# Kernel tuning notes

Measured on AMD Instinct MI355X. Metric: run time of the kernel, lower is better.

## Reference

```python
import jax, jax.numpy as jnp
import numpy as np
from jax import lax

K = 3
ALPHA = 2000.0
TAU = 0.001
MAX_ITER = 100
EPS = 1e-7


def setup_inputs() -> dict:
    key = jax.random.key(0)
    x = jax.random.normal(key, (8, 2048, 32), dtype=jnp.float32)
    return {"x": x}


def _vmd(x):
    B, L, D = x.shape
    # shifted frequency grid, identical across B and D
    f = jnp.fft.fftshift(jnp.fft.fftfreq(L)).astype(x.dtype)          # [L]
    f_bld = f[None, :, None]                                           # [1,L,1]
    # nonnegative-frequency mask; torch code boolean-masks f_shifted >= 0,
    # which is uniform over B and D, so it is a weighted sum over L here
    pos = (f >= 0).astype(x.dtype)[None, None, :, None]                # [1,1,L,1]
    x_hat = jnp.fft.fftshift(jnp.fft.fft(x, axis=1), axes=1)          # [B,L,D] complex

    def step(carry, _):
        u, omega, lam = carry  # u:[B,K,L,D], omega:[B,K,D], lam:[B,L,D]
        # Gauss-Seidel mode updates (each mode sees already-updated others)
        for k_idx in range(K):
            sum_other = jnp.sum(u, axis=1) - u[:, k_idx]               # [B,L,D]
            sum_other_hat = jnp.fft.fftshift(jnp.fft.fft(sum_other, axis=1), axes=1)
            num = x_hat - sum_other_hat + lam * 0.5                    # lam added in freq domain, as in source
            den = 1.0 + 2.0 * ALPHA * (f_bld - omega[:, k_idx][:, None, :]) ** 2
            u_k = jnp.real(jnp.fft.ifft(jnp.fft.ifftshift(num / den, axes=1), axis=1))
            u = u.at[:, k_idx].set(u_k)
        # center-frequency update over nonnegative shifted frequencies
        u_hat = jnp.fft.fftshift(jnp.fft.fft(u, axis=2), axes=2)       # [B,K,L,D]
        p = (u_hat.real ** 2 + u_hat.imag ** 2) * pos                  # |u_hat|^2 masked
        omega = jnp.sum(f[None, None, :, None] * p, axis=2) / (jnp.sum(p, axis=2) + EPS)  # [B,K,D]
        # dual ascent on lambda
        lam = lam + TAU * (x - jnp.sum(u, axis=1))
        return (u, omega, lam), None

    u0 = jnp.zeros((B, K, L, D), x.dtype)
    om0 = jnp.zeros((B, K, D), x.dtype)
    lam0 = jnp.zeros((B, L, D), x.dtype)
    (u, omega, _), _ = lax.scan(jax.checkpoint(step), (u0, om0, lam0), None, length=MAX_ITER)

    # sort modes per batch element by mean center frequency
    order = jnp.argsort(jnp.mean(omega, axis=2), axis=1)               # [B,K]
    u_sorted = jnp.take_along_axis(u, order[:, :, None, None], axis=1)
    return u_sorted[:, 0], u_sorted[:, 1], u_sorted[:, 2]


def reference(x):
    return _vmd(x)
```

## Files before the change

### kernel.cpp

```cpp
#include <hip/hip_runtime.h>

#define PD(i) ((i) + ((i) >> 5))
#define BLD 524288

__device__ __forceinline__ float2 cadd(float2 a, float2 b){ return make_float2(a.x+b.x, a.y+b.y); }
__device__ __forceinline__ float2 csub(float2 a, float2 b){ return make_float2(a.x-b.x, a.y-b.y); }
__device__ __forceinline__ float2 cmul(float2 a, float2 b){ return make_float2(a.x*b.x - a.y*b.y, a.x*b.y + a.y*b.x); }
__device__ __forceinline__ float2 cmuli(float2 a, float s){ return make_float2(-s*a.y, s*a.x); }

template<int SGN>
__device__ __forceinline__ void dft8(float2 a[8]) {
  const float sgn = (float)SGN;
  const float C8 = 0.70710678118654752440f;
  float2 e0=a[0], e1=a[2], e2=a[4], e3=a[6];
  float2 o0=a[1], o1=a[3], o2=a[5], o3=a[7];
  float2 t0=cadd(e0,e2), t1=csub(e0,e2), t2=cadd(e1,e3), t3=csub(e1,e3);
  float2 E0=cadd(t0,t2), E2=csub(t0,t2);
  float2 t3i=cmuli(t3,sgn);
  float2 E1=cadd(t1,t3i), E3=csub(t1,t3i);
  float2 s0=cadd(o0,o2), s1=csub(o0,o2), s2=cadd(o1,o3), s3=csub(o1,o3);
  float2 O0=cadd(s0,s2), O2=csub(s0,s2);
  float2 s3i=cmuli(s3,sgn);
  float2 O1=cadd(s1,s3i), O3=csub(s1,s3i);
  float2 w1o = make_float2(C8*(O1.x - sgn*O1.y), C8*(O1.y + sgn*O1.x));
  float2 w2o = cmuli(O2, sgn);
  float2 w3o = make_float2(-C8*(O3.x + sgn*O3.y), C8*(sgn*O3.x - O3.y));
  a[0]=cadd(E0,O0); a[4]=csub(E0,O0);
  a[1]=cadd(E1,w1o); a[5]=csub(E1,w1o);
  a[2]=cadd(E2,w2o); a[6]=csub(E2,w2o);
  a[3]=cadd(E3,w3o); a[7]=csub(E3,w3o);
}

template<int SGN>
__device__ void fft2048(float2* bufA, float2* bufB, const float2* twd, int tid)
{
  const float sgn = (float)SGN;
  {
    float2 a[8];
    #pragma unroll
    for (int j=0;j<8;j++) a[j] = bufA[PD(tid + 256*j)];
    dft8<SGN>(a);
    float2 tw = twd[tid];
    float2 w1 = make_float2(tw.x, sgn*tw.y), wj = w1;
    #pragma unroll
    for (int j=1;j<8;j++){ a[j] = cmul(a[j], wj); wj = cmul(wj, w1); }
    #pragma unroll
    for (int j=0;j<8;j++) bufB[PD(8*tid + j)] = a[j];
  }
  __syncthreads();
  {
    float2 a[8];
    #pragma unroll
    for (int j=0;j<8;j++) a[j] = bufB[PD(tid + 256*j)];
    dft8<SGN>(a);
    int p = tid >> 3, q = tid & 7;
    float2 tw = twd[p << 3];
    float2 w1 = make_float2(tw.x, sgn*tw.y), wj = w1;
    #pragma unroll
    for (int j=1;j<8;j++){ a[j] = cmul(a[j], wj); wj = cmul(wj, w1); }
    int base = q + (p << 6);
    #pragma unroll
    for (int j=0;j<8;j++) bufA[PD(base + (j<<3))] = a[j];
  }
  __syncthreads();
  {
    float2 a[8];
    #pragma unroll
    for (int j=0;j<8;j++) a[j] = bufA[PD(tid + 256*j)];
    dft8<SGN>(a);
    int p = tid >> 6, q = tid & 63;
    float2 tw = twd[p << 6];
    float2 w1 = make_float2(tw.x, sgn*tw.y), wj = w1;
    #pragma unroll
    for (int j=1;j<8;j++){ a[j] = cmul(a[j], wj); wj = cmul(wj, w1); }
    int base = q + (p << 9);
    #pragma unroll
    for (int j=0;j<8;j++) bufB[PD(base + (j<<6))] = a[j];
  }
  __syncthreads();
  {
    #pragma unroll
    for (int h=0; h<2; h++){
      int q = tid + (h<<8);
      float2 b0 = bufB[PD(q)], b1 = bufB[PD(q+512)], b2 = bufB[PD(q+1024)], b3 = bufB[PD(q+1536)];
      float2 t0=cadd(b0,b2), t1=csub(b0,b2), t2=cadd(b1,b3), t3=csub(b1,b3);
      float2 t3i=cmuli(t3,sgn);
      bufA[PD(q)]      = cadd(t0,t2);
      bufA[PD(q+512)]  = cadd(t1,t3i);
      bufA[PD(q+1024)] = csub(t0,t2);
      bufA[PD(q+1536)] = csub(t1,t3i);
    }
  }
  __syncthreads();
}

__device__ __forceinline__ void dft4p(float2 a[4]){
  float2 t0=cadd(a[0],a[2]), t1=csub(a[0],a[2]), t2=cadd(a[1],a[3]), t3=csub(a[1],a[3]);
  float2 t3i = make_float2(-t3.y, t3.x);
  a[0]=cadd(t0,t2); a[2]=csub(t0,t2);
  a[1]=cadd(t1,t3i); a[3]=csub(t1,t3i);
}

template<int S, int LS>
__device__ __forceinline__ void f1024_stage(const float2* __restrict__ in,
                                            float2* __restrict__ out,
                                            const float2* __restrict__ twd, int tid){
  float2 a[4];
  #pragma unroll
  for (int j=0;j<4;j++) a[j] = in[PD(tid + 256*j)];
  dft4p(a);
  if (S < 256) {
    int p = tid >> LS;
    int q = tid & (S-1);
    float2 w1 = twd[(2*S)*p];
    float2 w2 = cmul(w1,w1);
    float2 w3 = cmul(w2,w1);
    a[1]=cmul(a[1],w1); a[2]=cmul(a[2],w2); a[3]=cmul(a[3],w3);
    int base = q + 4*S*p;
    #pragma unroll
    for (int j=0;j<4;j++) out[PD(base + j*S)] = a[j];
  } else {
    #pragma unroll
    for (int j=0;j<4;j++) out[PD(tid + 256*j)] = a[j];
  }
}

__device__ void herm_fft_half(float2* __restrict__ A, float2* __restrict__ B,
                              const float2* __restrict__ twd, int tid){
  {
    float2 a[4];
    #pragma unroll
    for (int j=0;j<4;j++){
      int q = tid + 256*j;
      float2 lo = B[PD(q)], hi = B[PD(q+1024)];
      float2 Av = cadd(lo,hi), Bv = csub(lo,hi);
      float2 wq = twd[q];
      float2 WB = cmul(wq, Bv);
      a[j] = make_float2(Av.x - WB.y, Av.y + WB.x);
    }
    dft4p(a);
    float2 w1 = twd[2*tid];
    float2 w2 = cmul(w1,w1);
    float2 w3 = cmul(w2,w1);
    a[1]=cmul(a[1],w1); a[2]=cmul(a[2],w2); a[3]=cmul(a[3],w3);
    #pragma unroll
    for (int j=0;j<4;j++) A[PD(4*tid + j)] = a[j];
  }
  __syncthreads();
  f1024_stage<4,2>(A, B, twd, tid);   __syncthreads();
  f1024_stage<16,4>(B, A, twd, tid);  __syncthreads();
  f1024_stage<64,6>(A, B, twd, tid);  __syncthreads();
  f1024_stage<256,8>(B, A, twd, tid); __syncthreads();
}

template<bool TRANSP>
__global__ __launch_bounds__(256, 1) void vmd_main(const float* __restrict__ xg,
                                                   float* __restrict__ uout,
                                                   float* __restrict__ omout)
{
  __shared__ float2 sbufA[2112];
  __shared__ float2 sbufB[2112];
  __shared__ float2 stwd[1024];
  __shared__ float  sred[24];

  const int tid = threadIdx.x;
  const int blk = blockIdx.x;
  const int b = blk >> 5;
  const int d = blk & 31;
  const float inv2048 = 1.0f/2048.0f;

  for (int j = tid; j < 1024; j += 256) {
    double th = 3.14159265358979323846 * (double)j / 1024.0;
    stwd[j] = make_float2((float)cos(th), (float)sin(th));
  }

  int idxs[8];
  float fl[4], fh[4];
  #pragma unroll
  for (int c = 0; c < 4; c++) {
    int iL = 4*tid + c;
    idxs[c]   = iL;
    idxs[c+4] = (iL == 0) ? 1024 : (2048 - iL);
    fl[c] = (float)(idxs[c]   - 1024) * inv2048;
    fh[c] = (float)(idxs[c+4] - 1024) * inv2048;
  }

  float xv[8];
  #pragma unroll
  for (int e = 0; e < 8; e++) xv[e] = xg[(b*2048 + idxs[e])*32 + d];

  #pragma unroll
  for (int e = 0; e < 8; e++) {
    float v = (idxs[e] & 1) ? -xv[e] : xv[e];
    sbufA[PD(idxs[e])] = make_float2(v, 0.0f);
  }
  __syncthreads();
  fft2048<-1>(sbufA, sbufB, stwd, tid);
  float2 X[8];
  #pragma unroll
  for (int e = 0; e < 8; e++) X[e] = sbufA[PD(idxs[e])];

  float2 U[3][8];
  float2 S[8];
  float lam[8];
  #pragma unroll
  for (int e = 0; e < 8; e++) {
    S[e] = make_float2(0.f, 0.f); lam[e] = 0.f;
    #pragma unroll
    for (int k = 0; k < 3; k++) U[k][e] = make_float2(0.f, 0.f);
  }
  float om[3] = {0.f, 0.f, 0.f};
  const int wv = tid >> 6, ln = tid & 63;

  for (int iter = 0; iter < 100; iter++) {
    float xl[8];
    #pragma unroll
    for (int e = 0; e < 8; e++) xl[e] = fmaf(0.5f, lam[e], X[e].x);

    float sf[3], sp[3];
    #pragma unroll
    for (int k = 0; k < 3; k++) {
      sf[k] = 0.f; sp[k] = 0.f;
      #pragma unroll
      for (int c = 0; c < 4; c++) {
        float2 numl = make_float2(xl[c]     - S[c].x   + U[k][c].x,
                                  X[c].y    - S[c].y   + U[k][c].y);
        float2 numh = make_float2(xl[c+4]   - S[c+4].x + U[k][c+4].x,
                                  X[c+4].y  - S[c+4].y + U[k][c+4].y);
        float dl = fl[c] - om[k], dh = fh[c] - om[k];
        float rl = __builtin_amdgcn_rcpf(fmaf(4000.0f*dl, dl, 1.0f));
        float rh = __builtin_amdgcn_rcpf(fmaf(4000.0f*dh, dh, 1.0f));
        float2 Vl = make_float2(numl.x*rl, numl.y*rl);
        float2 Vh = make_float2(numh.x*rh, numh.y*rh);
        float2 Ul, Uh;
        if (tid == 0 && c == 0) {
          Ul = make_float2(Vl.x, 0.f);
          Uh = make_float2(Vh.x, 0.f);
        } else {
          Ul = make_float2(0.5f*(Vl.x + Vh.x), 0.5f*(Vl.y - Vh.y));
          Uh = make_float2(Ul.x, -Ul.y);
        }
        S[c].x   += Ul.x - U[k][c].x;   S[c].y   += Ul.y - U[k][c].y;
        S[c+4].x += Uh.x - U[k][c+4].x; S[c+4].y += Uh.y - U[k][c+4].y;
        U[k][c] = Ul; U[k][c+4] = Uh;
        float pw = Uh.x*Uh.x + Uh.y*Uh.y;
        sf[k] = fmaf(fh[c], pw, sf[k]);
        sp[k] += pw;
      }
    }

    #pragma unroll
    for (int e = 0; e < 8; e++) sbufB[PD(idxs[e])] = S[e];

    #pragma unroll
    for (int k = 0; k < 3; k++) {
      #pragma unroll
      for (int off = 32; off >= 1; off >>= 1) {
        sf[k] += __shfl_xor(sf[k], off);
        sp[k] += __shfl_xor(sp[k], off);
      }
    }
    if (ln == 0) {
      #pragma unroll
      for (int k = 0; k < 3; k++) { sred[wv*6 + k] = sf[k]; sred[wv*6 + 3 + k] = sp[k]; }
    }
    __syncthreads();

    #pragma unroll
    for (int k = 0; k < 3; k++) {
      float a = sred[k] + sred[6+k] + sred[12+k] + sred[18+k];
      float p = sred[3+k] + sred[9+k] + sred[15+k] + sred[21+k];
      om[k] = a / (p + 1e-7f);
    }

    herm_fft_half(sbufA, sbufB, stwd, tid);

    {
      float2 z0 = sbufA[PD(2*tid)];
      float2 z1 = sbufA[PD(2*tid+1)];
      int rh0 = (tid == 0) ? 512 : (1024 - 2*tid);
      float2 h0 = sbufA[PD(rh0)];
      float2 h1 = sbufA[PD(1023 - 2*tid)];
      float2 h2 = sbufA[PD(1022 - 2*tid)];
      float g[8];
      g[0]=z0.x; g[1]=z0.y; g[2]=z1.x; g[3]=z1.y;
      g[4]=h0.x; g[5]=h1.y; g[6]=h1.x; g[7]=h2.y;
      #pragma unroll
      for (int e = 0; e < 8; e++) {
        float sv = g[e] * inv2048;
        if (e & 1) sv = -sv;
        lam[e] = fmaf(0.001f, xv[e] - sv, lam[e]);
      }
    }
  }

  #pragma unroll
  for (int k = 0; k < 3; k++) {
    #pragma unroll
    for (int e = 0; e < 8; e++) sbufB[PD(idxs[e])] = U[k][e];
    __syncthreads();
    herm_fft_half(sbufA, sbufB, stwd, tid);
    {
      float2 z0 = sbufA[PD(2*tid)];
      float2 z1 = sbufA[PD(2*tid+1)];
      int rh0 = (tid == 0) ? 512 : (1024 - 2*tid);
      float2 h0 = sbufA[PD(rh0)];
      float2 h1 = sbufA[PD(1023 - 2*tid)];
      float2 h2 = sbufA[PD(1022 - 2*tid)];
      float g[8];
      g[0]=z0.x; g[1]=z0.y; g[2]=z1.x; g[3]=z1.y;
      g[4]=h0.x; g[5]=h1.y; g[6]=h1.x; g[7]=h2.y;
      #pragma unroll
      for (int e = 0; e < 8; e++) {
        float uv = g[e] * inv2048;
        if (e & 1) uv = -uv;
        if (TRANSP) uout[(((size_t)k*8 + b)*32 + d)*2048 + idxs[e]] = uv;
        else        uout[(size_t)k*BLD + ((size_t)b*2048 + idxs[e])*32 + d] = uv;
      }
    }
  }
  if (tid == 0) {
    omout[(b*3 + 0)*32 + d] = om[0];
    omout[(b*3 + 1)*32 + d] = om[1];
    omout[(b*3 + 2)*32 + d] = om[2];
  }
}

__global__ void vmd_order(const float* __restrict__ omout, int* __restrict__ ord)
{
  __shared__ float m[24];
  int t = threadIdx.x;
  if (t < 24) {
    float s = 0.f;
    for (int dd = 0; dd < 32; dd++) s += omout[t*32 + dd];
    m[t] = s;
  }
  __syncthreads();
  if (t < 8) {
    float v0 = m[t*3], v1 = m[t*3+1], v2 = m[t*3+2];
    int i0 = 0, i1 = 1, i2 = 2;
    if (v1 < v0){ float tv=v0; v0=v1; v1=tv; int ti=i0; i0=i1; i1=ti; }
    if (v2 < v1){ float tv=v1; v1=v2; v2=tv; int ti=i1; i1=i2; i2=ti; }
    if (v1 < v0){ float tv=v0; v0=v1; v1=tv; int ti=i0; i0=i1; i1=ti; }
    ord[t*3] = i0; ord[t*3+1] = i1; ord[t*3+2] = i2;
  }
}

__global__ __launch_bounds__(256) void vmd_permute(const float* __restrict__ wsu,
                                                   const int* __restrict__ ord,
                                                   float* __restrict__ out)
{
  __shared__ float tile[32][33];
  int bid = blockIdx.x;
  int lt = bid & 63;
  int b = (bid >> 6) & 7;
  int kpos = bid >> 9;
  int ks = ord[b*3 + kpos];
  int tr = threadIdx.x >> 5;
  int tc = threadIdx.x & 31;
  for (int it = 0; it < 4; it++) {
    int dd = tr + it*8;
    tile[dd][tc] = wsu[(((size_t)ks*8 + b)*32 + dd)*2048 + lt*32 + tc];
  }
  __syncthreads();
  for (int it = 0; it < 4; it++) {
    int ll = tr + it*8;
    out[(size_t)kpos*BLD + ((size_t)b*2048 + lt*32 + ll)*32 + tc] = tile[tc][ll];
  }
}

__global__ void vmd_inplace(float* __restrict__ out, const int* __restrict__ ord)
{
  int r = blockIdx.x * 256 + threadIdx.x;
  int b = r >> 16;
  int o0 = ord[b*3], o1 = ord[b*3+1], o2 = ord[b*3+2];
  float v0 = out[(size_t)o0*BLD + r];
  float v1 = out[(size_t)o1*BLD + r];
  float v2 = out[(size_t)o2*BLD + r];
  out[r] = v0;
  out[(size_t)BLD + r] = v1;
  out[(size_t)2*BLD + r] = v2;
}

extern "C" void kernel_launch(void* const* d_in, const int* in_sizes, int n_in,
                              void* d_out, int out_size, void* d_ws, size_t ws_size,
                              hipStream_t stream)
{
  const float* x = (const float*)d_in[0];
  float* out = (float*)d_out;
  const size_t NU = (size_t)3 * BLD;
  size_t need = NU*4 + 768*4 + 24*4;
  if (ws_size >= need) {
    float* wsu  = (float*)d_ws;
    float* wsom = wsu + NU;
    int*   wsord = (int*)(wsom + 768);
    vmd_main<true><<<256, 256, 0, stream>>>(x, wsu, wsom);
    vmd_order<<<1, 64, 0, stream>>>(wsom, wsord);
    vmd_permute<<<1536, 256, 0, stream>>>(wsu, wsord, out);
  } else {
    float* wsom = (float*)d_ws;
    int*   wsord = (int*)(wsom + 768);
    vmd_main<false><<<256, 256, 0, stream>>>(x, out, wsom);
    vmd_order<<<1, 64, 0, stream>>>(wsom, wsord);
    vmd_inplace<<<2048, 256, 0, stream>>>(out, wsord);
  }
}
```

Measured before the change: 339.8 us.

## Hoist FFT twiddles and indices, use DPP reductions, fold order kernel into permute

Precomputes per-thread LDS indices and stage twiddles once, outside the 100-iteration loop, so the inverse Hermitian FFT no longer reloads twiddles or recomputes addresses each iteration. Wave reductions switch from shuffles to DPP row operations, the omega division becomes a reciprocal multiply, and lambda is stored pre-halved to save a multiply. The separate ordering kernel is removed: each permute block recomputes the mode order itself, dropping one launch at the cost of redundant small reductions. The extra hoisted registers may raise register pressure.

```diff
diff --git a/kernel.cpp b/kernel.cpp
--- a/kernel.cpp
+++ b/kernel.cpp
@@ -7,6 +7,21 @@
 __device__ __forceinline__ float2 csub(float2 a, float2 b){ return make_float2(a.x-b.x, a.y-b.y); }
 __device__ __forceinline__ float2 cmul(float2 a, float2 b){ return make_float2(a.x*b.x - a.y*b.y, a.x*b.y + a.y*b.x); }
 __device__ __forceinline__ float2 cmuli(float2 a, float s){ return make_float2(-s*a.y, s*a.x); }
+
+template<int CTRL, int RM>
+__device__ __forceinline__ float dpp_add(float x){
+  int r = __builtin_amdgcn_update_dpp(0, __float_as_int(x), CTRL, RM, 0xf, true);
+  return x + __int_as_float(r);
+}
+__device__ __forceinline__ float wave_sum64(float x){
+  x = dpp_add<0x111,0xf>(x);
+  x = dpp_add<0x112,0xf>(x);
+  x = dpp_add<0x114,0xf>(x);
+  x = dpp_add<0x118,0xf>(x);
+  x = dpp_add<0x142,0xa>(x);
+  x = dpp_add<0x143,0xc>(x);
+  return x;
+}
 
 template<int SGN>
 __device__ __forceinline__ void dft8(float2 a[8]) {
@@ -101,58 +116,6 @@
   a[1]=cadd(t1,t3i); a[3]=csub(t1,t3i);
 }
 
-template<int S, int LS>
-__device__ __forceinline__ void f1024_stage(const float2* __restrict__ in,
-                                            float2* __restrict__ out,
-                                            const float2* __restrict__ twd, int tid){
-  float2 a[4];
-  #pragma unroll
-  for (int j=0;j<4;j++) a[j] = in[PD(tid + 256*j)];
-  dft4p(a);
-  if (S < 256) {
-    int p = tid >> LS;
-    int q = tid & (S-1);
-    float2 w1 = twd[(2*S)*p];
-    float2 w2 = cmul(w1,w1);
-    float2 w3 = cmul(w2,w1);
-    a[1]=cmul(a[1],w1); a[2]=cmul(a[2],w2); a[3]=cmul(a[3],w3);
-    int base = q + 4*S*p;
-    #pragma unroll
-    for (int j=0;j<4;j++) out[PD(base + j*S)] = a[j];
-  } else {
-    #pragma unroll
-    for (int j=0;j<4;j++) out[PD(tid + 256*j)] = a[j];
-  }
-}
-
-__device__ void herm_fft_half(float2* __restrict__ A, float2* __restrict__ B,
-                              const float2* __restrict__ twd, int tid){
-  {
-    float2 a[4];
-    #pragma unroll
-    for (int j=0;j<4;j++){
-      int q = tid + 256*j;
-      float2 lo = B[PD(q)], hi = B[PD(q+1024)];
-      float2 Av = cadd(lo,hi), Bv = csub(lo,hi);
-      float2 wq = twd[q];
-      float2 WB = cmul(wq, Bv);
-      a[j] = make_float2(Av.x - WB.y, Av.y + WB.x);
-    }
-    dft4p(a);
-    float2 w1 = twd[2*tid];
-    float2 w2 = cmul(w1,w1);
-    float2 w3 = cmul(w2,w1);
-    a[1]=cmul(a[1],w1); a[2]=cmul(a[2],w2); a[3]=cmul(a[3],w3);
-    #pragma unroll
-    for (int j=0;j<4;j++) A[PD(4*tid + j)] = a[j];
-  }
-  __syncthreads();
-  f1024_stage<4,2>(A, B, twd, tid);   __syncthreads();
-  f1024_stage<16,4>(B, A, twd, tid);  __syncthreads();
-  f1024_stage<64,6>(A, B, twd, tid);  __syncthreads();
-  f1024_stage<256,8>(B, A, twd, tid); __syncthreads();
-}
-
 template<bool TRANSP>
 __global__ __launch_bounds__(256, 1) void vmd_main(const float* __restrict__ xg,
                                                    float* __restrict__ uout,
@@ -184,6 +147,9 @@
     fl[c] = (float)(idxs[c]   - 1024) * inv2048;
     fh[c] = (float)(idxs[c+4] - 1024) * inv2048;
   }
+  int sI[8];
+  #pragma unroll
+  for (int e = 0; e < 8; e++) sI[e] = PD(idxs[e]);
 
   float xv[8];
   #pragma unroll
@@ -192,20 +158,106 @@
   #pragma unroll
   for (int e = 0; e < 8; e++) {
     float v = (idxs[e] & 1) ? -xv[e] : xv[e];
-    sbufA[PD(idxs[e])] = make_float2(v, 0.0f);
+    sbufA[sI[e]] = make_float2(v, 0.0f);
   }
   __syncthreads();
   fft2048<-1>(sbufA, sbufB, stwd, tid);
   float2 X[8];
   #pragma unroll
-  for (int e = 0; e < 8; e++) X[e] = sbufA[PD(idxs[e])];
+  for (int e = 0; e < 8; e++) X[e] = sbufA[sI[e]];
+
+  int rd[4]; float2 wq[4];
+  #pragma unroll
+  for (int j = 0; j < 4; j++) { int q = tid + 256*j; rd[j] = PD(q); wq[j] = stwd[q]; }
+  const int pw0 = PD(4*tid);
+  float2 c1w1 = stwd[2*tid];
+  float2 c1w2 = cmul(c1w1,c1w1), c1w3 = cmul(c1w2,c1w1);
+  float2 s4w1 = stwd[8*(tid>>2)];
+  float2 s4w2 = cmul(s4w1,s4w1), s4w3 = cmul(s4w2,s4w1);
+  float2 s16w1 = stwd[32*(tid>>4)];
+  float2 s16w2 = cmul(s16w1,s16w1), s16w3 = cmul(s16w2,s16w1);
+  float2 s64w1 = stwd[128*(tid>>6)];
+  float2 s64w2 = cmul(s64w1,s64w1), s64w3 = cmul(s64w2,s64w1);
+  int w4i[4], w16i[4], w64i[4];
+  { int base = (tid & 3) + ((tid>>2)<<4);
+    #pragma unroll
+    for (int j=0;j<4;j++) w4i[j]  = PD(base + (j<<2)); }
+  { int base = (tid & 15) + ((tid>>4)<<6);
+    #pragma unroll
+    for (int j=0;j<4;j++) w16i[j] = PD(base + (j<<4)); }
+  { int base = (tid & 63) + ((tid>>6)<<8);
+    #pragma unroll
+    for (int j=0;j<4;j++) w64i[j] = PD(base + (j<<6)); }
+  const int zi0 = PD(2*tid), zi1 = PD(2*tid+1);
+  const int zi2 = PD((tid==0) ? 512 : (1024 - 2*tid));
+  const int zi3 = PD(1023 - 2*tid), zi4 = PD(1022 - 2*tid);
+
+  auto herm = [&]() {
+    {
+      float2 C[4];
+      #pragma unroll
+      for (int j=0;j<4;j++){
+        float2 lo = sbufB[rd[j]];
+        float2 hi = sbufB[rd[j] + 1056];
+        float2 Av = cadd(lo,hi), Bv = csub(lo,hi);
+        float2 WB = cmul(wq[j], Bv);
+        C[j] = make_float2(Av.x - WB.y, Av.y + WB.x);
+      }
+      dft4p(C);
+      C[1]=cmul(C[1],c1w1); C[2]=cmul(C[2],c1w2); C[3]=cmul(C[3],c1w3);
+      sbufA[pw0]   = C[0];
+      sbufA[pw0+1] = C[1];
+      sbufA[pw0+2] = C[2];
+      sbufA[pw0+3] = C[3];
+    }
+    __syncthreads();
+    {
+      float2 a[4];
+      #pragma unroll
+      for (int j=0;j<4;j++) a[j] = sbufA[rd[j]];
+      dft4p(a);
+      a[1]=cmul(a[1],s4w1); a[2]=cmul(a[2],s4w2); a[3]=cmul(a[3],s4w3);
+      #pragma unroll
+      for (int j=0;j<4;j++) sbufB[w4i[j]] = a[j];
+    }
+    __syncthreads();
+    {
+      float2 a[4];
+      #pragma unroll
+      for (int j=0;j<4;j++) a[j] = sbufB[rd[j]];
+      dft4p(a);
+      a[1]=cmul(a[1],s16w1); a[2]=cmul(a[2],s16w2); a[3]=cmul(a[3],s16w3);
+      #pragma unroll
+      for (int j=0;j<4;j++) sbufA[w16i[j]] = a[j];
+    }
+    __syncthreads();
+    {
+      float2 a[4];
+      #pragma unroll
+      for (int j=0;j<4;j++) a[j] = sbufA[rd[j]];
+      dft4p(a);
+      a[1]=cmul(a[1],s64w1); a[2]=cmul(a[2],s64w2); a[3]=cmul(a[3],s64w3);
+      #pragma unroll
+      for (int j=0;j<4;j++) sbufB[w64i[j]] = a[j];
+    }
+    __syncthreads();
+    {
+      float2 a[4];
+      #pragma unroll
+      for (int j=0;j<4;j++) a[j] = sbufB[rd[j]];
+      dft4p(a);
+      #pragma unroll
+      for (int j=0;j<4;j++) sbufA[rd[j]] = a[j];
+    }
+    __syncthreads();
+  };
 
   float2 U[3][8];
   float2 S[8];
-  float lam[8];
+  float lam2[8];
   #pragma unroll
   for (int e = 0; e < 8; e++) {
-    S[e] = make_float2(0.f, 0.f); lam[e] = 0.f;
+    S[e] = make_float2(0.f, 0.f); lam2[e] = 0.f;
     #pragma unroll
     for (int k = 0; k < 3; k++) U[k][e] = make_float2(0.f, 0.f);
   }
@@ -215,7 +267,7 @@
   for (int iter = 0; iter < 100; iter++) {
     float xl[8];
     #pragma unroll
-    for (int e = 0; e < 8; e++) xl[e] = fmaf(0.5f, lam[e], X[e].x);
+    for (int e = 0; e < 8; e++) xl[e] = X[e].x + lam2[e];
 
     float sf[3], sp[3];
     #pragma unroll
@@ -250,17 +302,11 @@
     }
 
     #pragma unroll
-    for (int e = 0; e < 8; e++) sbufB[PD(idxs[e])] = S[e];
-
-    #pragma unroll
-    for (int k = 0; k < 3; k++) {
-      #pragma unroll
-      for (int off = 32; off >= 1; off >>= 1) {
-        sf[k] += __shfl_xor(sf[k], off);
-        sp[k] += __shfl_xor(sp[k], off);
-      }
-    }
-    if (ln == 0) {
+    for (int e = 0; e < 8; e++) sbufB[sI[e]] = S[e];
+
+    #pragma unroll
+    for (int k = 0; k < 3; k++) { sf[k] = wave_sum64(sf[k]); sp[k] = wave_sum64(sp[k]); }
+    if (ln == 63) {
       #pragma unroll
       for (int k = 0; k < 3; k++) { sred[wv*6 + k] = sf[k]; sred[wv*6 + 3 + k] = sp[k]; }
     }
@@ -270,18 +316,17 @@
     for (int k = 0; k < 3; k++) {
       float a = sred[k] + sred[6+k] + sred[12+k] + sred[18+k];
       float p = sred[3+k] + sred[9+k] + sred[15+k] + sred[21+k];
-      om[k] = a / (p + 1e-7f);
-    }
-
-    herm_fft_half(sbufA, sbufB, stwd, tid);
-
-    {
-      float2 z0 = sbufA[PD(2*tid)];
-      float2 z1 = sbufA[PD(2*tid+1)];
-      int rh0 = (tid == 0) ? 512 : (1024 - 2*tid);
-      float2 h0 = sbufA[PD(rh0)];
-      float2 h1 = sbufA[PD(1023 - 2*tid)];
-      float2 h2 = sbufA[PD(1022 - 2*tid)];
+      om[k] = a * __builtin_amdgcn_rcpf(p + 1e-7f);
+    }
+
+    herm();
+
+    {
+      float2 z0 = sbufA[zi0];
+      float2 z1 = sbufA[zi1];
+      float2 h0 = sbufA[zi2];
+      float2 h1 = sbufA[zi3];
+      float2 h2 = sbufA[zi4];
       float g[8];
       g[0]=z0.x; g[1]=z0.y; g[2]=z1.x; g[3]=z1.y;
       g[4]=h0.x; g[5]=h1.y; g[6]=h1.x; g[7]=h2.y;
@@ -289,7 +334,7 @@
       for (int e = 0; e < 8; e++) {
         float sv = g[e] * inv2048;
         if (e & 1) sv = -sv;
-        lam[e] = fmaf(0.001f, xv[e] - sv, lam[e]);
+        lam2[e] = fmaf(0.0005f, xv[e] - sv, lam2[e]);
       }
     }
   }
@@ -297,16 +342,15 @@
   #pragma unroll
   for (int k = 0; k < 3; k++) {
     #pragma unroll
-    for (int e = 0; e < 8; e++) sbufB[PD(idxs[e])] = U[k][e];
-    __syncthreads();
-    herm_fft_half(sbufA, sbufB, stwd, tid);
-    {
-      float2 z0 = sbufA[PD(2*tid)];
-      float2 z1 = sbufA[PD(2*tid+1)];
-      int rh0 = (tid == 0) ? 512 : (1024 - 2*tid);
-      float2 h0 = sbufA[PD(rh0)];
-      float2 h1 = sbufA[PD(1023 - 2*tid)];
-      float2 h2 = sbufA[PD(1022 - 2*tid)];
+    for (int e = 0; e < 8; e++) sbufB[sI[e]] = U[k][e];
+    __syncthreads();
+    herm();
+    {
+      float2 z0 = sbufA[zi0];
+      float2 z1 = sbufA[zi1];
+      float2 h0 = sbufA[zi2];
+      float2 h1 = sbufA[zi3];
+      float2 h2 = sbufA[zi4];
       float g[8];
       g[0]=z0.x; g[1]=z0.y; g[2]=z1.x; g[3]=z1.y;
       g[4]=h0.x; g[5]=h1.y; g[6]=h1.x; g[7]=h2.y;
@@ -326,38 +370,37 @@
   }
 }
 
-__global__ void vmd_order(const float* __restrict__ omout, int* __restrict__ ord)
-{
-  __shared__ float m[24];
-  int t = threadIdx.x;
-  if (t < 24) {
-    float s = 0.f;
-    for (int dd = 0; dd < 32; dd++) s += omout[t*32 + dd];
-    m[t] = s;
-  }
-  __syncthreads();
-  if (t < 8) {
-    float v0 = m[t*3], v1 = m[t*3+1], v2 = m[t*3+2];
-    int i0 = 0, i1 = 1, i2 = 2;
-    if (v1 < v0){ float tv=v0; v0=v1; v1=tv; int ti=i0; i0=i1; i1=ti; }
-    if (v2 < v1){ float tv=v1; v1=v2; v2=tv; int ti=i1; i1=i2; i2=ti; }
-    if (v1 < v0){ float tv=v0; v0=v1; v1=tv; int ti=i0; i0=i1; i1=ti; }
-    ord[t*3] = i0; ord[t*3+1] = i1; ord[t*3+2] = i2;
-  }
+__device__ __forceinline__ void order3(const float* sm, int* sord){
+  float v0=sm[0], v1=sm[1], v2=sm[2];
+  int j0=0,j1=1,j2=2;
+  if (v1<v0){float tv=v0;v0=v1;v1=tv;int ti=j0;j0=j1;j1=ti;}
+  if (v2<v1){float tv=v1;v1=v2;v2=tv;int ti=j1;j1=j2;j2=ti;}
+  if (v1<v0){float tv=v0;v0=v1;v1=tv;int ti=j0;j0=j1;j1=ti;}
+  sord[0]=j0; sord[1]=j1; sord[2]=j2;
 }
 
 __global__ __launch_bounds__(256) void vmd_permute(const float* __restrict__ wsu,
-                                                   const int* __restrict__ ord,
+                                                   const float* __restrict__ omout,
                                                    float* __restrict__ out)
 {
   __shared__ float tile[32][33];
+  __shared__ float sm[3];
+  __shared__ int sord[3];
   int bid = blockIdx.x;
   int lt = bid & 63;
   int b = (bid >> 6) & 7;
   int kpos = bid >> 9;
-  int ks = ord[b*3 + kpos];
-  int tr = threadIdx.x >> 5;
-  int tc = threadIdx.x & 31;
+  int tid = threadIdx.x;
+  if (tid < 3) {
+    float s = 0.f;
+    for (int dd = 0; dd < 32; dd++) s += omout[(b*3 + tid)*32 + dd];
+    sm[tid] = s;
+  }
+  __syncthreads();
+  if (tid == 0) order3(sm, sord);
+  __syncthreads();
+  int ks = sord[kpos];
+  int tr = tid >> 5, tc = tid & 31;
   for (int it = 0; it < 4; it++) {
     int dd = tr + it*8;
     tile[dd][tc] = wsu[(((size_t)ks*8 + b)*32 + dd)*2048 + lt*32 + tc];
@@ -369,11 +412,21 @@
   }
 }
 
-__global__ void vmd_inplace(float* __restrict__ out, const int* __restrict__ ord)
+__global__ void vmd_inplace(float* __restrict__ out, const float* __restrict__ omout)
 {
+  __shared__ float sm[3];
+  __shared__ int sord[3];
   int r = blockIdx.x * 256 + threadIdx.x;
   int b = r >> 16;
-  int o0 = ord[b*3], o1 = ord[b*3+1], o2 = ord[b*3+2];
+  if (threadIdx.x < 3) {
+    float s = 0.f;
+    for (int dd = 0; dd < 32; dd++) s += omout[(b*3 + threadIdx.x)*32 + dd];
+    sm[threadIdx.x] = s;
+  }
+  __syncthreads();
+  if (threadIdx.x == 0) order3(sm, sord);
+  __syncthreads();
+  int o0 = sord[0], o1 = sord[1], o2 = sord[2];
   float v0 = out[(size_t)o0*BLD + r];
   float v1 = out[(size_t)o1*BLD + r];
   float v2 = out[(size_t)o2*BLD + r];
@@ -389,19 +442,15 @@
   const float* x = (const float*)d_in[0];
   float* out = (float*)d_out;
   const size_t NU = (size_t)3 * BLD;
-  size_t need = NU*4 + 768*4 + 24*4;
+  size_t need = NU*4 + 768*4;
   if (ws_size >= need) {
     float* wsu  = (float*)d_ws;
     float* wsom = wsu + NU;
-    int*   wsord = (int*)(wsom + 768);
     vmd_main<true><<<256, 256, 0, stream>>>(x, wsu, wsom);
-    vmd_order<<<1, 64, 0, stream>>>(wsom, wsord);
-    vmd_permute<<<1536, 256, 0, stream>>>(wsu, wsord, out);
+    vmd_permute<<<1536, 256, 0, stream>>>(wsu, wsom, out);
   } else {
     float* wsom = (float*)d_ws;
-    int*   wsord = (int*)(wsom + 768);
     vmd_main<false><<<256, 256, 0, stream>>>(x, out, wsom);
-    vmd_order<<<1, 64, 0, stream>>>(wsom, wsord);
-    vmd_inplace<<<2048, 256, 0, stream>>>(out, wsord);
-  }
-}
+    vmd_inplace<<<2048, 256, 0, stream>>>(out, wsom);
+  }
+}
```

After: 313.2 us. -7.8%, faster.
